# Kernel tuning notes

Measured on AMD Instinct MI355X. Metric: run time of the kernel, lower is better.

Reference implementation:

```python
import jax, jax.numpy as jnp
import numpy as np

D_SCALED = 8  # adaptive pool output spatial size


def setup_inputs() -> dict:
    key = jax.random.key(0)
    ks = jax.random.split(key, 5)
    b, t, c, h, w = 8, 16, 64, 56, 56
    d_t = 16
    d_in = D_SCALED * D_SCALED  # 64
    d_out = d_t * 2             # 32
    return {
        "x": jax.random.normal(ks[0], (b, t, c, h, w), dtype=jnp.float32),
        "Wq": jax.random.normal(ks[1], (d_in, d_out), dtype=jnp.float32) * 0.001,
        "bq": jax.random.normal(ks[2], (d_out,), dtype=jnp.float32) * 0.001,
        "Wk": jax.random.normal(ks[3], (d_in, d_out), dtype=jnp.float32) * 0.001,
        "bk": jax.random.normal(ks[4], (d_out,), dtype=jnp.float32) * 0.001,
    }


def reference(x, Wq, bq, Wk, bk):
    b, t, c, h, w = x.shape
    ds = D_SCALED
    # shift_x: [b, c, t, h, w]
    shift = jnp.transpose(x, (0, 2, 1, 3, 4))
    # AdaptiveAvgPool3d((None, ds, ds)): h,w divide evenly -> reshape-mean
    pooled = shift.reshape(b, c, t, ds, h // ds, ds, w // ds).mean(axis=(4, 6))
    flat = pooled.reshape(b * c, t, ds * ds)          # [bc, t, ds*ds]
    q = flat @ Wq + bq                                # [bc, t, 2*d_t]
    k = flat @ Wk + bk                                # [bc, t, 2*d_t]
    att = jnp.einsum('ntd,nsd->nts', q, k) / np.sqrt(t).astype(jnp.float32)
    att = jax.nn.softmax(att, axis=-1)                # [bc, t, t]
    v = shift.reshape(b * c, t, h * w)                # [bc, t, h*w]
    out = jnp.einsum('nts,nsv->ntv', att, v)          # [bc, t, h*w]
    out = out.reshape(b, c, t, h, w)
    return jnp.transpose(out, (0, 2, 1, 3, 4))        # [b, t, c, h, w]
```

## Files before the change

### kernel.cpp

```cpp
#include <hip/hip_runtime.h>
#include <math.h>

#define B  8
#define T  16
#define C  64
#define H  56
#define W  56
#define HW (H*W)
#define HW4 (HW/4)
#define DS 8
#define DIN (DS*DS)
#define DOUT 32
#define BC (B*C)
#define GSL 2
#define NGRP (T/GSL)

typedef float vfloat4 __attribute__((ext_vector_type(4)));

__global__ __launch_bounds__(256, 4) void fused_kernel(const float* __restrict__ x,
                                                       const float* __restrict__ Wq,
                                                       const float* __restrict__ bq,
                                                       const float* __restrict__ Wk,
                                                       const float* __restrict__ bk,
                                                       float* __restrict__ out) {
    __shared__ float xs[GSL * HW];
    __shared__ float pooled_s[T * DIN];
    __shared__ float qs[T * 33];
    __shared__ float ks[T * 33];
    __shared__ float att_s[T * T];
    __shared__ float att_tr[T * T];

    const int n = blockIdx.x;
    const int tid = threadIdx.x;
    const int b = n >> 6;
    const int c = n & 63;

    const float4* x4 = (const float4*)x;
    float4* xs4 = (float4*)xs;

    #pragma unroll 1
    for (int g = 0; g < NGRP; ++g) {
        for (int i = tid; i < GSL * HW4; i += 256) {
            const int ti = (i >= HW4) ? 1 : 0;
            const int p  = i - ti * HW4;
            xs4[i] = x4[((size_t)(b * T + g * GSL + ti) * C + c) * HW4 + p];
        }
        __syncthreads();
        if (tid < GSL * 64) {
            const int ti  = tid >> 6;
            const int wi  = tid & 63;
            const int ri  = wi >> 3;
            const int rj  = wi & 7;
            float s = 0.f;
            const int base = ti * HW + (7 * ri) * W + 7 * rj;
            #pragma unroll
            for (int di = 0; di < 7; ++di) {
                #pragma unroll
                for (int dj = 0; dj < 7; ++dj) s += xs[base + di * W + dj];
            }
            pooled_s[(g * GSL + ti) * DIN + wi] = s * (1.0f / 49.0f);
        }
        __syncthreads();
    }

    for (int e = tid; e < T * DOUT; e += 256) {
        const int t = e >> 5;
        const int d = e & 31;
        float sq = bq[d];
        float sk = bk[d];
        #pragma unroll 8
        for (int kk = 0; kk < DIN; ++kk) {
            const float f = pooled_s[t * DIN + kk];
            sq = fmaf(f, Wq[kk * DOUT + d], sq);
            sk = fmaf(f, Wk[kk * DOUT + d], sk);
        }
        qs[t * 33 + d] = sq;
        ks[t * 33 + d] = sk;
    }
    __syncthreads();

    {
        const int tt = tid >> 4;
        const int ss = tid & 15;
        float s = 0.f;
        #pragma unroll
        for (int d = 0; d < DOUT; ++d) s = fmaf(qs[tt * 33 + d], ks[ss * 33 + d], s);
        att_s[tid] = s * 0.25f;
    }
    __syncthreads();

    if (tid < T) {
        const int r = tid;
        float m = -INFINITY;
        #pragma unroll
        for (int s = 0; s < T; ++s) m = fmaxf(m, att_s[r * T + s]);
        float e[T];
        float sum = 0.f;
        #pragma unroll
        for (int s = 0; s < T; ++s) { e[s] = __expf(att_s[r * T + s] - m); sum += e[s]; }
        const float inv = 1.0f / sum;
        #pragma unroll
        for (int s = 0; s < T; ++s) att_tr[s * T + r] = e[s] * inv;
    }
    __syncthreads();

    const float4* att4 = (const float4*)att_tr;
    float4* o4 = (float4*)out;
    const size_t xbase = ((size_t)(b * T) * C + c) * HW4;
    const size_t tstride = (size_t)C * HW4;

    #pragma unroll 1
    for (int i = tid; i < HW4; i += 256) {
        float4 acc[16];
        #pragma unroll
        for (int t = 0; t < 16; ++t) acc[t] = make_float4(0.f, 0.f, 0.f, 0.f);

        #pragma unroll 4
        for (int s = 0; s < T; ++s) {
            const float4 xv = x4[xbase + (size_t)s * tstride + i];
            #pragma unroll
            for (int q = 0; q < 4; ++q) {
                const float4 a = att4[s * 4 + q];
                acc[q*4+0].x = fmaf(a.x, xv.x, acc[q*4+0].x);
                acc[q*4+0].y = fmaf(a.x, xv.y, acc[q*4+0].y);
                acc[q*4+0].z = fmaf(a.x, xv.z, acc[q*4+0].z);
                acc[q*4+0].w = fmaf(a.x, xv.w, acc[q*4+0].w);
                acc[q*4+1].x = fmaf(a.y, xv.x, acc[q*4+1].x);
                acc[q*4+1].y = fmaf(a.y, xv.y, acc[q*4+1].y);
                acc[q*4+1].z = fmaf(a.y, xv.z, acc[q*4+1].z);
                acc[q*4+1].w = fmaf(a.y, xv.w, acc[q*4+1].w);
                acc[q*4+2].x = fmaf(a.z, xv.x, acc[q*4+2].x);
                acc[q*4+2].y = fmaf(a.z, xv.y, acc[q*4+2].y);
                acc[q*4+2].z = fmaf(a.z, xv.z, acc[q*4+2].z);
                acc[q*4+2].w = fmaf(a.z, xv.w, acc[q*4+2].w);
                acc[q*4+3].x = fmaf(a.w, xv.x, acc[q*4+3].x);
                acc[q*4+3].y = fmaf(a.w, xv.y, acc[q*4+3].y);
                acc[q*4+3].z = fmaf(a.w, xv.z, acc[q*4+3].z);
                acc[q*4+3].w = fmaf(a.w, xv.w, acc[q*4+3].w);
            }
        }

        #pragma unroll
        for (int t = 0; t < 16; ++t) {
            vfloat4* dst = (vfloat4*)&o4[xbase + (size_t)t * tstride + i];
            vfloat4 v; v.x = acc[t].x; v.y = acc[t].y; v.z = acc[t].z; v.w = acc[t].w;
            __builtin_nontemporal_store(v, dst);
        }
    }
}

extern "C" void kernel_launch(void* const* d_in, const int* in_sizes, int n_in,
                              void* d_out, int out_size, void* d_ws, size_t ws_size,
                              hipStream_t stream) {
    const float* x  = (const float*)d_in[0];
    const float* Wq = (const float*)d_in[1];
    const float* bq = (const float*)d_in[2];
    const float* Wk = (const float*)d_in[3];
    const float* bk = (const float*)d_in[4];
    float* out = (float*)d_out;

    fused_kernel<<<dim3(BC), dim3(256), 0, stream>>>(x, Wq, bq, Wk, bk, out);
}
```

Baseline: 220.3 us.

## Split fused kernel into pool, attention, and apply kernels with more parallelism

Replaces the single per-(b,c) fused kernel with three launches. Pooling runs on a (BC,T) grid with the row reduction split across four wave groups. Attention is computed per (b,c) into a workspace buffer, and the apply step runs on a (BC,7) grid where each wave produces 8 output timesteps. The aim is more blocks and more overlap than 512 large serialized blocks, at the cost of launch overhead and reading x twice. The pooled intermediates are staged in the output buffer, which apply_kernel later overwrites.

```diff
diff --git a/kernel.cpp b/kernel.cpp
--- a/kernel.cpp
+++ b/kernel.cpp
@@ -12,56 +12,67 @@
 #define DIN (DS*DS)
 #define DOUT 32
 #define BC (B*C)
-#define GSL 2
-#define NGRP (T/GSL)
 
 typedef float vfloat4 __attribute__((ext_vector_type(4)));
 
-__global__ __launch_bounds__(256, 4) void fused_kernel(const float* __restrict__ x,
-                                                       const float* __restrict__ Wq,
-                                                       const float* __restrict__ bq,
-                                                       const float* __restrict__ Wk,
-                                                       const float* __restrict__ bk,
-                                                       float* __restrict__ out) {
-    __shared__ float xs[GSL * HW];
-    __shared__ float pooled_s[T * DIN];
-    __shared__ float qs[T * 33];
-    __shared__ float ks[T * 33];
-    __shared__ float att_s[T * T];
-    __shared__ float att_tr[T * T];
 
+__global__ __launch_bounds__(256) void pool_kernel(const float* __restrict__ x,
+                                                   float* __restrict__ pooled_g) {
+    __shared__ float xs[HW];
+    __shared__ float part[256];
     const int n = blockIdx.x;
+    const int t = blockIdx.y;
     const int tid = threadIdx.x;
     const int b = n >> 6;
     const int c = n & 63;
 
     const float4* x4 = (const float4*)x;
     float4* xs4 = (float4*)xs;
+    const size_t base = ((size_t)(b * T + t) * C + c) * HW4;
 
-    #pragma unroll 1
-    for (int g = 0; g < NGRP; ++g) {
-        for (int i = tid; i < GSL * HW4; i += 256) {
-            const int ti = (i >= HW4) ? 1 : 0;
-            const int p  = i - ti * HW4;
-            xs4[i] = x4[((size_t)(b * T + g * GSL + ti) * C + c) * HW4 + p];
+    for (int i = tid; i < HW4; i += 256) xs4[i] = x4[base + i];
+    __syncthreads();
+
+    {
+        const int wi = tid & 63;
+        const int q  = tid >> 6;
+        const int ri = wi >> 3;
+        const int rj = wi & 7;
+        const int r0 = 2 * q;
+        const int nrows = (q < 3) ? 2 : 1;
+        float s = 0.f;
+        for (int dr = 0; dr < nrows; ++dr) {
+            const int row = 7 * ri + r0 + dr;
+            const int col0 = 7 * rj;
+            #pragma unroll
+            for (int dj = 0; dj < 7; ++dj) s += xs[row * W + col0 + dj];
         }
-        __syncthreads();
-        if (tid < GSL * 64) {
-            const int ti  = tid >> 6;
-            const int wi  = tid & 63;
-            const int ri  = wi >> 3;
-            const int rj  = wi & 7;
-            float s = 0.f;
-            const int base = ti * HW + (7 * ri) * W + 7 * rj;
-            #pragma unroll
-            for (int di = 0; di < 7; ++di) {
-                #pragma unroll
-                for (int dj = 0; dj < 7; ++dj) s += xs[base + di * W + dj];
-            }
-            pooled_s[(g * GSL + ti) * DIN + wi] = s * (1.0f / 49.0f);
-        }
-        __syncthreads();
+        part[q * 64 + wi] = s;
     }
+    __syncthreads();
+
+    if (tid < 64) {
+        const float v = part[tid] + part[tid + 64] + part[tid + 128] + part[tid + 192];
+        pooled_g[((size_t)n * T + t) * DIN + tid] = v * (1.0f / 49.0f);
+    }
+}
+
+__global__ __launch_bounds__(256) void att_kernel(const float* __restrict__ pooled_g,
+                                                  const float* __restrict__ Wq,
+                                                  const float* __restrict__ bq,
+                                                  const float* __restrict__ Wk,
+                                                  const float* __restrict__ bk,
+                                                  float* __restrict__ att_g) {
+    __shared__ float pooled_s[T * DIN];
+    __shared__ float qs[T * 33];
+    __shared__ float ks[T * 33];
+    __shared__ float att_s[T * T];
+
+    const int n = blockIdx.x;
+    const int tid = threadIdx.x;
+
+    for (int e = tid; e < T * DIN; e += 256) pooled_s[e] = pooled_g[(size_t)n * (T * DIN) + e];
+    __syncthreads();
 
     for (int e = tid; e < T * DOUT; e += 256) {
         const int t = e >> 5;
@@ -100,49 +111,51 @@
         for (int s = 0; s < T; ++s) { e[s] = __expf(att_s[r * T + s] - m); sum += e[s]; }
         const float inv = 1.0f / sum;
         #pragma unroll
-        for (int s = 0; s < T; ++s) att_tr[s * T + r] = e[s] * inv;
+        for (int s = 0; s < T; ++s) att_g[(size_t)n * (T * T) + r * T + s] = e[s] * inv;
     }
+}
+
+__global__ __launch_bounds__(128) void apply_kernel(const float* __restrict__ x,
+                                                    const float* __restrict__ att_g,
+                                                    float* __restrict__ out) {
+    __shared__ float att_s[T * T];
+    const int n = blockIdx.x;
+    const int chunk = blockIdx.y;
+    const int tid = threadIdx.x;
+    const int lane = tid & 63;
+    const int wave = tid >> 6;
+    const int b = n >> 6;
+    const int c = n & 63;
+
+    for (int e = tid; e < T * T; e += 128) att_s[e] = att_g[(size_t)n * (T * T) + e];
     __syncthreads();
 
-    const float4* att4 = (const float4*)att_tr;
+    const float4* x4 = (const float4*)x;
     float4* o4 = (float4*)out;
-    const size_t xbase = ((size_t)(b * T) * C + c) * HW4;
-    const size_t tstride = (size_t)C * HW4;
 
     #pragma unroll 1
-    for (int i = tid; i < HW4; i += 256) {
-        float4 acc[16];
+    for (int i = lane; i < 112; i += 64) {
+        const int p4 = chunk * 112 + i;
+        float4 acc[8];
         #pragma unroll
-        for (int t = 0; t < 16; ++t) acc[t] = make_float4(0.f, 0.f, 0.f, 0.f);
+        for (int t = 0; t < 8; ++t) acc[t] = make_float4(0.f, 0.f, 0.f, 0.f);
 
-        #pragma unroll 4
+        #pragma unroll 8
         for (int s = 0; s < T; ++s) {
-            const float4 xv = x4[xbase + (size_t)s * tstride + i];
+            const float4 xv = x4[((size_t)(b * T + s) * C + c) * HW4 + p4];
             #pragma unroll
-            for (int q = 0; q < 4; ++q) {
-                const float4 a = att4[s * 4 + q];
-                acc[q*4+0].x = fmaf(a.x, xv.x, acc[q*4+0].x);
-                acc[q*4+0].y = fmaf(a.x, xv.y, acc[q*4+0].y);
-                acc[q*4+0].z = fmaf(a.x, xv.z, acc[q*4+0].z);
-                acc[q*4+0].w = fmaf(a.x, xv.w, acc[q*4+0].w);
-                acc[q*4+1].x = fmaf(a.y, xv.x, acc[q*4+1].x);
-                acc[q*4+1].y = fmaf(a.y, xv.y, acc[q*4+1].y);
-                acc[q*4+1].z = fmaf(a.y, xv.z, acc[q*4+1].z);
-                acc[q*4+1].w = fmaf(a.y, xv.w, acc[q*4+1].w);
-                acc[q*4+2].x = fmaf(a.z, xv.x, acc[q*4+2].x);
-                acc[q*4+2].y = fmaf(a.z, xv.y, acc[q*4+2].y);
-                acc[q*4+2].z = fmaf(a.z, xv.z, acc[q*4+2].z);
-                acc[q*4+2].w = fmaf(a.z, xv.w, acc[q*4+2].w);
-                acc[q*4+3].x = fmaf(a.w, xv.x, acc[q*4+3].x);
-                acc[q*4+3].y = fmaf(a.w, xv.y, acc[q*4+3].y);
-                acc[q*4+3].z = fmaf(a.w, xv.z, acc[q*4+3].z);
-                acc[q*4+3].w = fmaf(a.w, xv.w, acc[q*4+3].w);
+            for (int t = 0; t < 8; ++t) {
+                const float a = att_s[(wave * 8 + t) * T + s];
+                acc[t].x = fmaf(a, xv.x, acc[t].x);
+                acc[t].y = fmaf(a, xv.y, acc[t].y);
+                acc[t].z = fmaf(a, xv.z, acc[t].z);
+                acc[t].w = fmaf(a, xv.w, acc[t].w);
             }
         }
 
         #pragma unroll
-        for (int t = 0; t < 16; ++t) {
-            vfloat4* dst = (vfloat4*)&o4[xbase + (size_t)t * tstride + i];
+        for (int t = 0; t < 8; ++t) {
+            vfloat4* dst = (vfloat4*)&o4[((size_t)(b * T + wave * 8 + t) * C + c) * HW4 + p4];
             vfloat4 v; v.x = acc[t].x; v.y = acc[t].y; v.z = acc[t].z; v.w = acc[t].w;
             __builtin_nontemporal_store(v, dst);
         }
@@ -159,5 +172,10 @@
     const float* bk = (const float*)d_in[4];
     float* out = (float*)d_out;
 
-    fused_kernel<<<dim3(BC), dim3(256), 0, stream>>>(x, Wq, bq, Wk, bk, out);
+    float* pooled_g = out;
+    float* att_g = (float*)d_ws;
+
+    pool_kernel<<<dim3(BC, T), dim3(256), 0, stream>>>(x, pooled_g);
+    att_kernel<<<dim3(BC), dim3(256), 0, stream>>>(pooled_g, Wq, bq, Wk, bk, att_g);
+    apply_kernel<<<dim3(BC, 7), dim3(128), 0, stream>>>(x, att_g, out);
 }
```

Result: faster. 211.7 us (-3.9%).

## Restructure fused kernel to 1024 threads with 14-row chunks staged in LDS

Applied to the files above, without the earlier changes.

Each block now uses 1024 threads. Both the pooling pass and the attention-apply pass walk the image in four 14-row chunks covering all 16 time steps, staged in shared memory (about 50 KB). Pooling splits rows across four thread quarters and reduces the partial sums through a shared buffer. The output pass reads x from LDS and gives each thread a single float4 output instead of 16 register accumulators, and nontemporal stores are replaced by plain stores. The aim is higher parallelism and lower register pressure, at the cost of more syncs, more LDS traffic, and large LDS per block that limits occupancy.

```diff
diff --git a/kernel.cpp b/kernel.cpp
--- a/kernel.cpp
+++ b/kernel.cpp
@@ -8,25 +8,23 @@
 #define W  56
 #define HW (H*W)
 #define HW4 (HW/4)
-#define DS 8
-#define DIN (DS*DS)
+#define CHUNK 196
+#define NCHUNK 4
+#define DIN 64
 #define DOUT 32
 #define BC (B*C)
-#define GSL 2
-#define NGRP (T/GSL)
 
-typedef float vfloat4 __attribute__((ext_vector_type(4)));
-
-__global__ __launch_bounds__(256, 4) void fused_kernel(const float* __restrict__ x,
-                                                       const float* __restrict__ Wq,
-                                                       const float* __restrict__ bq,
-                                                       const float* __restrict__ Wk,
-                                                       const float* __restrict__ bk,
-                                                       float* __restrict__ out) {
-    __shared__ float xs[GSL * HW];
+__global__ __launch_bounds__(1024, 8) void fused_kernel(const float* __restrict__ x,
+                                                        const float* __restrict__ Wq,
+                                                        const float* __restrict__ bq,
+                                                        const float* __restrict__ Wk,
+                                                        const float* __restrict__ bk,
+                                                        float* __restrict__ out) {
+    __shared__ float xs[16 * (CHUNK * 4)];
+    __shared__ float part[1024];
     __shared__ float pooled_s[T * DIN];
     __shared__ float qs[T * 33];
-    __shared__ float ks[T * 33];
+    __shared__ float ksh[T * 33];
     __shared__ float att_s[T * T];
     __shared__ float att_tr[T * T];
 
@@ -36,36 +34,50 @@
     const int c = n & 63;
 
     const float4* x4 = (const float4*)x;
+    float4* o4 = (float4*)out;
     float4* xs4 = (float4*)xs;
+    const size_t base = ((size_t)(b * T) * C + c) * HW4;
+    const size_t tstr = (size_t)C * HW4;
 
     #pragma unroll 1
-    for (int g = 0; g < NGRP; ++g) {
-        for (int i = tid; i < GSL * HW4; i += 256) {
-            const int ti = (i >= HW4) ? 1 : 0;
-            const int p  = i - ti * HW4;
-            xs4[i] = x4[((size_t)(b * T + g * GSL + ti) * C + c) * HW4 + p];
+    for (int g = 0; g < NCHUNK; ++g) {
+        for (int i = tid; i < 16 * CHUNK; i += 1024) {
+            const int s   = i / CHUNK;
+            const int off = i - s * CHUNK;
+            xs4[i] = x4[base + (size_t)s * tstr + g * CHUNK + off];
         }
         __syncthreads();
-        if (tid < GSL * 64) {
-            const int ti  = tid >> 6;
-            const int wi  = tid & 63;
-            const int ri  = wi >> 3;
-            const int rj  = wi & 7;
+        {
+            const int q  = tid >> 8;
+            const int wi = tid & 255;
+            const int sl = wi >> 4;
+            const int w8 = wi & 15;
+            const int wrow = w8 >> 3;
+            const int wcol = w8 & 7;
+            const int r0 = 2 * q;
+            const int nr = (q < 3) ? 2 : 1;
             float s = 0.f;
-            const int base = ti * HW + (7 * ri) * W + 7 * rj;
-            #pragma unroll
-            for (int di = 0; di < 7; ++di) {
+            for (int dr = 0; dr < nr; ++dr) {
+                const int row = wrow * 7 + r0 + dr;
+                const int fbase = sl * (CHUNK * 4) + row * W + wcol * 7;
                 #pragma unroll
-                for (int dj = 0; dj < 7; ++dj) s += xs[base + di * W + dj];
+                for (int j = 0; j < 7; ++j) s += xs[fbase + j];
             }
-            pooled_s[(g * GSL + ti) * DIN + wi] = s * (1.0f / 49.0f);
+            part[q * 256 + wi] = s;
+        }
+        __syncthreads();
+        if (tid < 256) {
+            const int sl = tid >> 4;
+            const int w8 = tid & 15;
+            const float v = part[tid] + part[tid + 256] + part[tid + 512] + part[tid + 768];
+            pooled_s[sl * DIN + g * 16 + w8] = v * (1.0f / 49.0f);
         }
         __syncthreads();
     }
 
-    for (int e = tid; e < T * DOUT; e += 256) {
-        const int t = e >> 5;
-        const int d = e & 31;
+    if (tid < T * DOUT) {
+        const int t = tid >> 5;
+        const int d = tid & 31;
         float sq = bq[d];
         float sk = bk[d];
         #pragma unroll 8
@@ -75,16 +87,16 @@
             sk = fmaf(f, Wk[kk * DOUT + d], sk);
         }
         qs[t * 33 + d] = sq;
-        ks[t * 33 + d] = sk;
+        ksh[t * 33 + d] = sk;
     }
     __syncthreads();
 
-    {
+    if (tid < T * T) {
         const int tt = tid >> 4;
         const int ss = tid & 15;
         float s = 0.f;
         #pragma unroll
-        for (int d = 0; d < DOUT; ++d) s = fmaf(qs[tt * 33 + d], ks[ss * 33 + d], s);
+        for (int d = 0; d < DOUT; ++d) s = fmaf(qs[tt * 33 + d], ksh[ss * 33 + d], s);
         att_s[tid] = s * 0.25f;
     }
     __syncthreads();
@@ -104,48 +116,30 @@
     }
     __syncthreads();
 
-    const float4* att4 = (const float4*)att_tr;
-    float4* o4 = (float4*)out;
-    const size_t xbase = ((size_t)(b * T) * C + c) * HW4;
-    const size_t tstride = (size_t)C * HW4;
-
     #pragma unroll 1
-    for (int i = tid; i < HW4; i += 256) {
-        float4 acc[16];
-        #pragma unroll
-        for (int t = 0; t < 16; ++t) acc[t] = make_float4(0.f, 0.f, 0.f, 0.f);
-
-        #pragma unroll 4
-        for (int s = 0; s < T; ++s) {
-            const float4 xv = x4[xbase + (size_t)s * tstride + i];
-            #pragma unroll
-            for (int q = 0; q < 4; ++q) {
-                const float4 a = att4[s * 4 + q];
-                acc[q*4+0].x = fmaf(a.x, xv.x, acc[q*4+0].x);
-                acc[q*4+0].y = fmaf(a.x, xv.y, acc[q*4+0].y);
-                acc[q*4+0].z = fmaf(a.x, xv.z, acc[q*4+0].z);
-                acc[q*4+0].w = fmaf(a.x, xv.w, acc[q*4+0].w);
-                acc[q*4+1].x = fmaf(a.y, xv.x, acc[q*4+1].x);
-                acc[q*4+1].y = fmaf(a.y, xv.y, acc[q*4+1].y);
-                acc[q*4+1].z = fmaf(a.y, xv.z, acc[q*4+1].z);
-                acc[q*4+1].w = fmaf(a.y, xv.w, acc[q*4+1].w);
-                acc[q*4+2].x = fmaf(a.z, xv.x, acc[q*4+2].x);
-                acc[q*4+2].y = fmaf(a.z, xv.y, acc[q*4+2].y);
-                acc[q*4+2].z = fmaf(a.z, xv.z, acc[q*4+2].z);
-                acc[q*4+2].w = fmaf(a.z, xv.w, acc[q*4+2].w);
-                acc[q*4+3].x = fmaf(a.w, xv.x, acc[q*4+3].x);
-                acc[q*4+3].y = fmaf(a.w, xv.y, acc[q*4+3].y);
-                acc[q*4+3].z = fmaf(a.w, xv.z, acc[q*4+3].z);
-                acc[q*4+3].w = fmaf(a.w, xv.w, acc[q*4+3].w);
+    for (int g = 0; g < NCHUNK; ++g) {
+        for (int i = tid; i < 16 * CHUNK; i += 1024) {
+            const int s   = i / CHUNK;
+            const int off = i - s * CHUNK;
+            xs4[i] = x4[base + (size_t)s * tstr + g * CHUNK + off];
+        }
+        __syncthreads();
+        for (int i = tid; i < 16 * CHUNK; i += 1024) {
+            const int t   = i / CHUNK;
+            const int col = i - t * CHUNK;
+            float4 a = make_float4(0.f, 0.f, 0.f, 0.f);
+            #pragma unroll 4
+            for (int s = 0; s < T; ++s) {
+                const float w = att_tr[s * T + t];
+                const float4 xv = xs4[s * CHUNK + col];
+                a.x = fmaf(w, xv.x, a.x);
+                a.y = fmaf(w, xv.y, a.y);
+                a.z = fmaf(w, xv.z, a.z);
+                a.w = fmaf(w, xv.w, a.w);
             }
+            o4[base + (size_t)t * tstr + g * CHUNK + col] = a;
         }
-
-        #pragma unroll
-        for (int t = 0; t < 16; ++t) {
-            vfloat4* dst = (vfloat4*)&o4[xbase + (size_t)t * tstride + i];
-            vfloat4 v; v.x = acc[t].x; v.y = acc[t].y; v.z = acc[t].z; v.w = acc[t].w;
-            __builtin_nontemporal_store(v, dst);
-        }
+        __syncthreads();
     }
 }
 
@@ -159,5 +153,5 @@
     const float* bk = (const float*)d_in[4];
     float* out = (float*)d_out;
 
-    fused_kernel<<<dim3(BC), dim3(256), 0, stream>>>(x, Wq, bq, Wk, bk, out);
+    fused_kernel<<<dim3(BC), dim3(1024), 0, stream>>>(x, Wq, bq, Wk, bk, out);
 }
```

After: 208.4 us. 5.4% less time.
